# Kernel optimization log

Measured on AMD Instinct MI355X. Metric: run time of the kernel, lower is better.

Reference implementation:

```python
import jax, jax.numpy as jnp
import numpy as np

B, N, EDGES = 16, 50000, 1600000
CLAMP_MIN, CLAMP_MAX = -10.0, 10.0
EPS = 1e-6


def setup_inputs() -> dict:
    key = jax.random.key(0)
    ks = jax.random.split(key, 8)
    return {
        "chem_influence": jax.random.normal(ks[0], (B, N), dtype=jnp.float32),
        "E": jax.random.normal(ks[1], (B, N), dtype=jnp.float32),
        "o_pre": jax.random.uniform(ks[2], (B, N), dtype=jnp.float32),
        "w": jax.random.normal(ks[3], (EDGES,), dtype=jnp.float32),
        "threshold": jax.random.uniform(ks[4], (N,), dtype=jnp.float32),
        "decay": jax.random.uniform(ks[5], (N,), dtype=jnp.float32),
        "src": jax.random.randint(ks[6], (EDGES,), 0, N, dtype=jnp.int32),
        "dst": jax.random.randint(ks[7], (EDGES,), 0, N, dtype=jnp.int32),
    }


def reference(chem_influence, E, o_pre, w, threshold, decay, src, dst):
    # Gap-junction currents: gather, sign-compare, weighted scatter-add.
    Oj = o_pre[:, src]                      # (B, EDGES) presynaptic outputs
    En = E[:, dst]                          # (B, EDGES) postsynaptic internal states
    sgn = jnp.where(Oj >= En, 1.0, -1.0)
    contrib = Oj * w * sgn                  # (B, EDGES)
    gj_sum = jnp.zeros_like(chem_influence).at[:, dst].add(contrib)  # (B, N)

    # Neuron dynamics (eqs 10, 11).
    S = jnp.clip(E + chem_influence + gj_sum, CLAMP_MIN, CLAMP_MAX)
    gt = S > threshold                      # broadcast (N,) over (B, N)
    mask = (~gt) & (jnp.abs(S - E) <= EPS)
    new_o = jax.nn.relu(S - threshold)
    new_e = jnp.where(gt, new_o, jnp.where(mask, E - decay, S))
    return (new_o, new_e)
```

## Files before the change

### kernel.cpp

```cpp
#include <hip/hip_runtime.h>

#define BATCH 16
#define NNODES 50000
#define NEDGES 1600000
#define BN (BATCH * NNODES)
#define NBLK 196
#define EPB 8192
#define BSZ 128
#define NBINS 391
#define CAPE 4992
#define CLAMP_LO -10.0f
#define CLAMP_HI 10.0f
#define EPS_V 1e-6f

__global__ void prep_hist_kernel(const float* __restrict__ o_pre,
                                 const float* __restrict__ E,
                                 const int* __restrict__ dst,
                                 float* __restrict__ o_t,
                                 float* __restrict__ E_t,
                                 int* __restrict__ hist) {
    __shared__ int lh[NBINS];
    const int tid = threadIdx.x, bid = blockIdx.x;
    for (int i = tid; i < NBINS; i += 256) lh[i] = 0;

    int t = bid * 256 + tid;
    if (t < NNODES) {
        float v[BATCH], u[BATCH];
#pragma unroll
        for (int b = 0; b < BATCH; ++b) {
            v[b] = o_pre[b * NNODES + t];
            u[b] = E[b * NNODES + t];
        }
        float4* op = (float4*)(o_t + (size_t)t * BATCH);
        float4* ep = (float4*)(E_t + (size_t)t * BATCH);
#pragma unroll
        for (int k = 0; k < 4; ++k) {
            op[k] = make_float4(v[4 * k], v[4 * k + 1], v[4 * k + 2], v[4 * k + 3]);
            ep[k] = make_float4(u[4 * k], u[4 * k + 1], u[4 * k + 2], u[4 * k + 3]);
        }
    }
    __syncthreads();

    const int4* dst4 = (const int4*)dst;
    const int e4base = bid * (EPB / 4);
#pragma unroll
    for (int j = 0; j < 8; ++j) {
        int i4 = e4base + j * 256 + tid;
        if (i4 * 4 < NEDGES) {
            int4 d4 = dst4[i4];
            atomicAdd(&lh[d4.x >> 7], 1);
            atomicAdd(&lh[d4.y >> 7], 1);
            atomicAdd(&lh[d4.z >> 7], 1);
            atomicAdd(&lh[d4.w >> 7], 1);
        }
    }
    __syncthreads();
    for (int i = tid; i < NBINS; i += 256) hist[i * NBLK + bid] = lh[i];
}

__global__ void scanA_kernel(int* __restrict__ hist, int* __restrict__ totals) {
    __shared__ int sm[256];
    int k = blockIdx.x, t = threadIdx.x;
    int v = (t < NBLK) ? hist[k * NBLK + t] : 0;
    sm[t] = v;
    __syncthreads();
    for (int off = 1; off < 256; off <<= 1) {
        int a = (t >= off) ? sm[t - off] : 0;
        __syncthreads();
        sm[t] += a;
        __syncthreads();
    }
    if (t < NBLK) hist[k * NBLK + t] = sm[t] - v;
    if (t == 0) totals[k] = sm[255];
}

__global__ void scatterA_kernel(const int* __restrict__ src,
                                const int* __restrict__ dst,
                                const float* __restrict__ w,
                                const int* __restrict__ hist,
                                uint2* __restrict__ binned) {
    __shared__ int cur[NBINS];
    const int tid = threadIdx.x, bid = blockIdx.x;
    for (int i = tid; i < NBINS; i += 256)
        cur[i] = i * CAPE + hist[i * NBLK + bid];
    __syncthreads();
    const int4*   dst4 = (const int4*)dst;
    const int4*   src4 = (const int4*)src;
    const float4* w4   = (const float4*)w;
    const int e4base = bid * (EPB / 4);
#pragma unroll
    for (int j = 0; j < 8; ++j) {
        int i4 = e4base + j * 256 + tid;
        if (i4 * 4 < NEDGES) {
            int4 d4 = dst4[i4];
            int4 s4 = src4[i4];
            float4 ww = w4[i4];
            int dd[4] = {d4.x, d4.y, d4.z, d4.w};
            int ss[4] = {s4.x, s4.y, s4.z, s4.w};
            float wv[4] = {ww.x, ww.y, ww.z, ww.w};
#pragma unroll
            for (int m = 0; m < 4; ++m) {
                int d = dd[m];
                int bin = d >> 7;
                int pos = atomicAdd(&cur[bin], 1);
                if (pos < (bin + 1) * CAPE)
                    binned[pos] = make_uint2(
                        (unsigned)ss[m] | ((unsigned)(d & 127) << 16),
                        __float_as_uint(wv[m]));
            }
        }
    }
}

__global__ __launch_bounds__(512) void bin_gather2(
    const float* __restrict__ o_t,
    const float* __restrict__ E_t,
    const float* __restrict__ chem,
    const float* __restrict__ threshold,
    const float* __restrict__ decay,
    const int* __restrict__ totals,
    const uint2* __restrict__ binned,
    float* __restrict__ out_o,
    float* __restrict__ out_e) {
    __shared__ int   cnt_l[BSZ];
    __shared__ int   offs[BSZ + 1];
    __shared__ int   sc[BSZ];
    __shared__ uint2 eb[CAPE];

    const int k = blockIdx.x, tid = threadIdx.x;
    const int node0 = k * BSZ;
    const int nn = (NNODES - node0 < BSZ) ? (NNODES - node0) : BSZ;
    const int s0 = k * CAPE;
    int cnt = totals[k];
    if (cnt > CAPE) cnt = CAPE;
    const int s1 = s0 + cnt;

    if (tid < BSZ) cnt_l[tid] = 0;
    __syncthreads();
    for (int i = s0 + tid; i < s1; i += 512)
        atomicAdd(&cnt_l[(binned[i].x >> 16) & 127], 1);
    __syncthreads();

    if (tid < BSZ) sc[tid] = cnt_l[tid];
    __syncthreads();
    for (int o = 1; o < BSZ; o <<= 1) {
        int v = (tid >= o && tid < BSZ) ? sc[tid - o] : 0;
        __syncthreads();
        if (tid < BSZ) sc[tid] += v;
        __syncthreads();
    }
    if (tid < BSZ) {
        int ex = sc[tid] - cnt_l[tid];
        offs[tid] = ex;
        cnt_l[tid] = ex;
    }
    if (tid == 0) offs[BSZ] = cnt;
    __syncthreads();

    for (int i = s0 + tid; i < s1; i += 512) {
        uint2 p = binned[i];
        int pos = atomicAdd(&cnt_l[(p.x >> 16) & 127], 1);
        if (pos < CAPE) eb[pos] = p;
    }
    __syncthreads();

    for (int t = tid; t < nn * 4; t += 512) {
        int n = t >> 2;
        int q = (t & 3) * 4;
        int gn = node0 + n;
        int e0 = offs[n], e1 = offs[n + 1];
        float4 en = *(const float4*)(E_t + (size_t)gn * BATCH + q);
        float4 acc = make_float4(0.f, 0.f, 0.f, 0.f);
        for (int i = e0; i < e1; ++i) {
            uint2 p = eb[i];
            float wv = __uint_as_float(p.y);
            int s = (int)(p.x & 0xFFFFu);
            float4 oj = *(const float4*)(o_t + (size_t)s * BATCH + q);
            acc.x += (oj.x >= en.x) ? oj.x * wv : -oj.x * wv;
            acc.y += (oj.y >= en.y) ? oj.y * wv : -oj.y * wv;
            acc.z += (oj.z >= en.z) ? oj.z * wv : -oj.z * wv;
            acc.w += (oj.w >= en.w) ? oj.w * wv : -oj.w * wv;
        }
        float th = threshold[gn];
        float dc = decay[gn];
        float ev[4] = {en.x, en.y, en.z, en.w};
        float av[4] = {acc.x, acc.y, acc.z, acc.w};
#pragma unroll
        for (int j = 0; j < 4; ++j) {
            int b = q + j;
            float e = ev[j];
            float S = e + chem[b * NNODES + gn] + av[j];
            S = fminf(fmaxf(S, CLAMP_LO), CLAMP_HI);
            float no = fmaxf(S - th, 0.0f);
            float ne;
            if (S > th) ne = no;
            else if (fabsf(S - e) <= EPS_V) ne = e - dc;
            else ne = S;
            out_o[b * NNODES + gn] = no;
            out_e[b * NNODES + gn] = ne;
        }
    }
}

__global__ void edge_scatter_dev(const float* __restrict__ o_pre, const float* __restrict__ E,
                                 const float* __restrict__ w, const int* __restrict__ src,
                                 const int* __restrict__ dst, float* __restrict__ gj) {
    int e = blockIdx.x * blockDim.x + threadIdx.x;
    if (e >= NEDGES) return;
    int s = src[e];
    int d = dst[e];
    float wv = w[e];
#pragma unroll
    for (int b = 0; b < BATCH; ++b) {
        float oj = o_pre[b * NNODES + s];
        float en = E[b * NNODES + d];
        atomicAdd(&gj[b * NNODES + d], (oj >= en) ? oj * wv : -oj * wv);
    }
}

__global__ void finalize_dev(const float* __restrict__ chem, const float* __restrict__ E,
                             const float* __restrict__ threshold, const float* __restrict__ decay,
                             float* __restrict__ out_o, float* __restrict__ out_e_gj) {
    int i = blockIdx.x * blockDim.x + threadIdx.x;
    if (i >= BN) return;
    int n = i % NNODES;
    float e = E[i];
    float S = e + chem[i] + out_e_gj[i];
    S = fminf(fmaxf(S, CLAMP_LO), CLAMP_HI);
    float th = threshold[n];
    float no = fmaxf(S - th, 0.0f);
    float ne;
    if (S > th) ne = no;
    else if (fabsf(S - e) <= EPS_V) ne = e - decay[n];
    else ne = S;
    out_o[i] = no;
    out_e_gj[i] = ne;
}

extern "C" void kernel_launch(void* const* d_in, const int* in_sizes, int n_in,
                              void* d_out, int out_size, void* d_ws, size_t ws_size,
                              hipStream_t stream) {
    const float* chem      = (const float*)d_in[0];
    const float* E         = (const float*)d_in[1];
    const float* o_pre     = (const float*)d_in[2];
    const float* w         = (const float*)d_in[3];
    const float* threshold = (const float*)d_in[4];
    const float* decay     = (const float*)d_in[5];
    const int*   src       = (const int*)d_in[6];
    const int*   dst       = (const int*)d_in[7];

    float* out_o = (float*)d_out;
    float* out_e = (float*)d_out + BN;

    const size_t OT_OFF  = 0;
    const size_t ET_OFF  = 3200000;
    const size_t BIN_OFF = 6400000;
    const size_t H_OFF   = 22014976;
    const size_t TOT_OFF = 22321536;
    const size_t need    = TOT_OFF + (size_t)NBINS * sizeof(int);

    if (ws_size >= need) {
        char* ws = (char*)d_ws;
        float* o_t    = (float*)(ws + OT_OFF);
        float* E_t    = (float*)(ws + ET_OFF);
        uint2* binned = (uint2*)(ws + BIN_OFF);
        int*   hist   = (int*)(ws + H_OFF);
        int*   totals = (int*)(ws + TOT_OFF);

        prep_hist_kernel<<<NBLK, 256, 0, stream>>>(o_pre, E, dst, o_t, E_t, hist);
        scanA_kernel<<<NBINS, 256, 0, stream>>>(hist, totals);
        scatterA_kernel<<<NBLK, 256, 0, stream>>>(src, dst, w, hist, binned);
        bin_gather2<<<NBINS, 512, 0, stream>>>(o_t, E_t, chem, threshold, decay,
                                               totals, binned, out_o, out_e);
    } else {
        hipMemsetAsync(out_e, 0, (size_t)BN * sizeof(float), stream);
        edge_scatter_dev<<<(NEDGES + 255) / 256, 256, 0, stream>>>(o_pre, E, w, src, dst, out_e);
        finalize_dev<<<(BN + 255) / 256, 256, 0, stream>>>(chem, E, threshold, decay, out_o, out_e);
    }
}
```

Before: 132.3 us.

## Fuse four-kernel binning pipeline into one persistent kernel with grid barriers

Replaces the histogram, scan, scatter and gather kernels with a single persistent kernel of 782 blocks that syncs through software grid barriers on global atomic counters. Bins shrink to 64 nodes each, and E is kept transposed in shared memory rather than written to a workspace. The aim is to remove three kernel launch gaps and the E_t round trip. The cost is spin-wait barriers and a per-call occupancy query on the host. It relies on all blocks being co-resident, which the occupancy check only partly guards, and the hist matrix is much larger (782x782).

```diff
diff --git a/kernel.cpp b/kernel.cpp
--- a/kernel.cpp
+++ b/kernel.cpp
@@ -4,14 +4,211 @@
 #define NNODES 50000
 #define NEDGES 1600000
 #define BN (BATCH * NNODES)
+#define CLAMP_LO -10.0f
+#define CLAMP_HI 10.0f
+#define EPS_V 1e-6f
+
+#define GRID2 782
+#define BSZ2 64
+#define CAPE2 2560
+#define EPB2 2048
+
 #define NBLK 196
 #define EPB 8192
 #define BSZ 128
 #define NBINS 391
 #define CAPE 4992
-#define CLAMP_LO -10.0f
-#define CLAMP_HI 10.0f
-#define EPS_V 1e-6f
+
+__device__ __forceinline__ void grid_barrier(int* ctr) {
+    __syncthreads();
+    if (threadIdx.x == 0) {
+        __threadfence();
+        atomicAdd(ctr, 1);
+        while (__hip_atomic_load(ctr, __ATOMIC_RELAXED, __HIP_MEMORY_SCOPE_AGENT) < GRID2) {
+            __builtin_amdgcn_s_sleep(1);
+        }
+        __threadfence();
+    }
+    __syncthreads();
+}
+
+__global__ __launch_bounds__(256, 4) void fused_all(
+    const float* __restrict__ o_pre, const float* __restrict__ E,
+    const int* __restrict__ src, const int* __restrict__ dst,
+    const float* __restrict__ w, const float* __restrict__ chem,
+    const float* __restrict__ threshold, const float* __restrict__ decay,
+    float* __restrict__ o_t, uint2* __restrict__ binned,
+    int* __restrict__ hist, int* __restrict__ totals, int* __restrict__ bars,
+    float* __restrict__ out_o, float* __restrict__ out_e) {
+    __shared__ __align__(16) char smem_raw[21264];
+    __shared__ float Et_l[BSZ2 * BATCH];
+    int*   lh    = (int*)smem_raw;
+    int*   sm    = (int*)smem_raw;
+    int*   cur   = (int*)smem_raw;
+    uint2* eb    = (uint2*)smem_raw;
+    int*   cnt_l = (int*)(smem_raw + 20480);
+    int*   offs  = (int*)(smem_raw + 20736);
+    int*   sc    = (int*)(smem_raw + 20996);
+
+    const int k = blockIdx.x, tid = threadIdx.x;
+    const int node0 = k * BSZ2;
+    const int nn = (NNODES - node0 < BSZ2) ? (NNODES - node0) : BSZ2;
+
+    for (int i = tid; i < GRID2; i += 256) lh[i] = 0;
+    for (int i = tid; i < BSZ2 * BATCH; i += 256) {
+        int b = i >> 6, n = i & 63;
+        if (n < nn) {
+            o_t[(size_t)(node0 + n) * BATCH + b] = o_pre[b * NNODES + node0 + n];
+            Et_l[n * BATCH + b] = E[b * NNODES + node0 + n];
+        }
+    }
+    __syncthreads();
+    const int4* dst4 = (const int4*)dst;
+#pragma unroll
+    for (int j = 0; j < 2; ++j) {
+        int i4 = k * (EPB2 / 4) + j * 256 + tid;
+        if (i4 * 4 < NEDGES) {
+            int4 d4 = dst4[i4];
+            atomicAdd(&lh[d4.x >> 6], 1);
+            atomicAdd(&lh[d4.y >> 6], 1);
+            atomicAdd(&lh[d4.z >> 6], 1);
+            atomicAdd(&lh[d4.w >> 6], 1);
+        }
+    }
+    __syncthreads();
+    for (int i = tid; i < GRID2; i += 256) hist[(size_t)i * GRID2 + k] = lh[i];
+    grid_barrier(&bars[0]);
+
+    {
+        int* row = hist + (size_t)k * GRID2;
+        int base = tid * 4;
+        int v[4];
+        int psum = 0;
+#pragma unroll
+        for (int j = 0; j < 4; ++j) {
+            int idx = base + j;
+            v[j] = (idx < GRID2) ? row[idx] : 0;
+            psum += v[j];
+        }
+        sm[tid] = psum;
+        __syncthreads();
+        for (int off = 1; off < 256; off <<= 1) {
+            int a = (tid >= off) ? sm[tid - off] : 0;
+            __syncthreads();
+            sm[tid] += a;
+            __syncthreads();
+        }
+        int run = (tid > 0) ? sm[tid - 1] : 0;
+#pragma unroll
+        for (int j = 0; j < 4; ++j) {
+            int idx = base + j;
+            if (idx < GRID2) { row[idx] = run; run += v[j]; }
+        }
+        if (tid == 0) totals[k] = sm[255];
+    }
+    grid_barrier(&bars[1]);
+
+    for (int i = tid; i < GRID2; i += 256)
+        cur[i] = i * CAPE2 + hist[(size_t)i * GRID2 + k];
+    __syncthreads();
+    {
+        const int4*   src4 = (const int4*)src;
+        const float4* w4   = (const float4*)w;
+#pragma unroll
+        for (int j = 0; j < 2; ++j) {
+            int i4 = k * (EPB2 / 4) + j * 256 + tid;
+            if (i4 * 4 < NEDGES) {
+                int4 d4 = dst4[i4];
+                int4 s4 = src4[i4];
+                float4 ww = w4[i4];
+                int dd[4] = {d4.x, d4.y, d4.z, d4.w};
+                int ss[4] = {s4.x, s4.y, s4.z, s4.w};
+                float wv[4] = {ww.x, ww.y, ww.z, ww.w};
+#pragma unroll
+                for (int m = 0; m < 4; ++m) {
+                    int d = dd[m];
+                    int bin = d >> 6;
+                    int pos = atomicAdd(&cur[bin], 1);
+                    if (pos < (bin + 1) * CAPE2)
+                        binned[pos] = make_uint2(
+                            (unsigned)ss[m] | ((unsigned)(d & 63) << 16),
+                            __float_as_uint(wv[m]));
+                }
+            }
+        }
+    }
+    grid_barrier(&bars[2]);
+
+    const int s0 = k * CAPE2;
+    int cnt = totals[k];
+    if (cnt > CAPE2) cnt = CAPE2;
+    const int s1 = s0 + cnt;
+
+    if (tid < BSZ2) cnt_l[tid] = 0;
+    __syncthreads();
+    for (int i = s0 + tid; i < s1; i += 256)
+        atomicAdd(&cnt_l[(binned[i].x >> 16) & 63], 1);
+    __syncthreads();
+    if (tid < BSZ2) sc[tid] = cnt_l[tid];
+    __syncthreads();
+    for (int o = 1; o < BSZ2; o <<= 1) {
+        int v = (tid >= o && tid < BSZ2) ? sc[tid - o] : 0;
+        __syncthreads();
+        if (tid < BSZ2) sc[tid] += v;
+        __syncthreads();
+    }
+    if (tid < BSZ2) {
+        int ex = sc[tid] - cnt_l[tid];
+        offs[tid] = ex;
+        cnt_l[tid] = ex;
+    }
+    if (tid == 0) offs[BSZ2] = cnt;
+    __syncthreads();
+    for (int i = s0 + tid; i < s1; i += 256) {
+        uint2 p = binned[i];
+        int pos = atomicAdd(&cnt_l[(p.x >> 16) & 63], 1);
+        if (pos < CAPE2) eb[pos] = p;
+    }
+    __syncthreads();
+
+    if (tid < nn * 4) {
+        int n = tid >> 2;
+        int q = (tid & 3) * 4;
+        int gn = node0 + n;
+        int e0 = offs[n], e1 = offs[n + 1];
+        float4 en = *(const float4*)(Et_l + n * BATCH + q);
+        float4 acc = make_float4(0.f, 0.f, 0.f, 0.f);
+        for (int i = e0; i < e1; ++i) {
+            uint2 p = eb[i];
+            float wv = __uint_as_float(p.y);
+            int s = (int)(p.x & 0xFFFFu);
+            float4 oj = *(const float4*)(o_t + (size_t)s * BATCH + q);
+            acc.x += (oj.x >= en.x) ? oj.x * wv : -oj.x * wv;
+            acc.y += (oj.y >= en.y) ? oj.y * wv : -oj.y * wv;
+            acc.z += (oj.z >= en.z) ? oj.z * wv : -oj.z * wv;
+            acc.w += (oj.w >= en.w) ? oj.w * wv : -oj.w * wv;
+        }
+        float th = threshold[gn];
+        float dc = decay[gn];
+        float ev[4] = {en.x, en.y, en.z, en.w};
+        float av[4] = {acc.x, acc.y, acc.z, acc.w};
+#pragma unroll
+        for (int j = 0; j < 4; ++j) {
+            int b = q + j;
+            float e = ev[j];
+            float S = e + chem[b * NNODES + gn] + av[j];
+            S = fminf(fmaxf(S, CLAMP_LO), CLAMP_HI);
+            float no = fmaxf(S - th, 0.0f);
+            float ne;
+            if (S > th) ne = no;
+            else if (fabsf(S - e) <= EPS_V) ne = e - dc;
+            else ne = S;
+            out_o[b * NNODES + gn] = no;
+            out_e[b * NNODES + gn] = ne;
+        }
+    }
+}
+
 
 __global__ void prep_hist_kernel(const float* __restrict__ o_pre,
                                  const float* __restrict__ E,
@@ -22,7 +219,6 @@
     __shared__ int lh[NBINS];
     const int tid = threadIdx.x, bid = blockIdx.x;
     for (int i = tid; i < NBINS; i += 256) lh[i] = 0;
-
     int t = bid * 256 + tid;
     if (t < NNODES) {
         float v[BATCH], u[BATCH];
@@ -34,13 +230,12 @@
         float4* op = (float4*)(o_t + (size_t)t * BATCH);
         float4* ep = (float4*)(E_t + (size_t)t * BATCH);
 #pragma unroll
-        for (int k = 0; k < 4; ++k) {
-            op[k] = make_float4(v[4 * k], v[4 * k + 1], v[4 * k + 2], v[4 * k + 3]);
-            ep[k] = make_float4(u[4 * k], u[4 * k + 1], u[4 * k + 2], u[4 * k + 3]);
-        }
-    }
-    __syncthreads();
-
+        for (int kk = 0; kk < 4; ++kk) {
+            op[kk] = make_float4(v[4 * kk], v[4 * kk + 1], v[4 * kk + 2], v[4 * kk + 3]);
+            ep[kk] = make_float4(u[4 * kk], u[4 * kk + 1], u[4 * kk + 2], u[4 * kk + 3]);
+        }
+    }
+    __syncthreads();
     const int4* dst4 = (const int4*)dst;
     const int e4base = bid * (EPB / 4);
 #pragma unroll
@@ -113,20 +308,15 @@
 }
 
 __global__ __launch_bounds__(512) void bin_gather2(
-    const float* __restrict__ o_t,
-    const float* __restrict__ E_t,
-    const float* __restrict__ chem,
-    const float* __restrict__ threshold,
-    const float* __restrict__ decay,
-    const int* __restrict__ totals,
+    const float* __restrict__ o_t, const float* __restrict__ E_t,
+    const float* __restrict__ chem, const float* __restrict__ threshold,
+    const float* __restrict__ decay, const int* __restrict__ totals,
     const uint2* __restrict__ binned,
-    float* __restrict__ out_o,
-    float* __restrict__ out_e) {
+    float* __restrict__ out_o, float* __restrict__ out_e) {
     __shared__ int   cnt_l[BSZ];
     __shared__ int   offs[BSZ + 1];
     __shared__ int   sc[BSZ];
     __shared__ uint2 eb[CAPE];
-
     const int k = blockIdx.x, tid = threadIdx.x;
     const int node0 = k * BSZ;
     const int nn = (NNODES - node0 < BSZ) ? (NNODES - node0) : BSZ;
@@ -134,13 +324,11 @@
     int cnt = totals[k];
     if (cnt > CAPE) cnt = CAPE;
     const int s1 = s0 + cnt;
-
     if (tid < BSZ) cnt_l[tid] = 0;
     __syncthreads();
     for (int i = s0 + tid; i < s1; i += 512)
         atomicAdd(&cnt_l[(binned[i].x >> 16) & 127], 1);
     __syncthreads();
-
     if (tid < BSZ) sc[tid] = cnt_l[tid];
     __syncthreads();
     for (int o = 1; o < BSZ; o <<= 1) {
@@ -156,14 +344,12 @@
     }
     if (tid == 0) offs[BSZ] = cnt;
     __syncthreads();
-
     for (int i = s0 + tid; i < s1; i += 512) {
         uint2 p = binned[i];
         int pos = atomicAdd(&cnt_l[(p.x >> 16) & 127], 1);
         if (pos < CAPE) eb[pos] = p;
     }
     __syncthreads();
-
     for (int t = tid; t < nn * 4; t += 512) {
         int n = t >> 2;
         int q = (t & 3) * 4;
@@ -252,21 +438,42 @@
     float* out_o = (float*)d_out;
     float* out_e = (float*)d_out + BN;
 
+    const size_t F_OT  = 0;
+    const size_t F_BIN = 3200000;
+    const size_t F_H   = 19215360;
+    const size_t F_TOT = 21661456;
+    const size_t F_BAR = 21664592;
+    const size_t need_f = F_BAR + 16;
+
     const size_t OT_OFF  = 0;
     const size_t ET_OFF  = 3200000;
     const size_t BIN_OFF = 6400000;
     const size_t H_OFF   = 22014976;
     const size_t TOT_OFF = 22321536;
-    const size_t need    = TOT_OFF + (size_t)NBINS * sizeof(int);
-
-    if (ws_size >= need) {
+    const size_t need2   = TOT_OFF + (size_t)NBINS * sizeof(int);
+
+    int blocksPerCU = 0;
+    hipError_t oe = hipOccupancyMaxActiveBlocksPerMultiprocessor(&blocksPerCU, fused_all, 256, 0);
+    bool coop_ok = (oe == hipSuccess) && ((long)blocksPerCU * 256 >= GRID2) && (ws_size >= need_f);
+
+    if (coop_ok) {
+        char* ws = (char*)d_ws;
+        float* o_t    = (float*)(ws + F_OT);
+        uint2* binned = (uint2*)(ws + F_BIN);
+        int*   hist   = (int*)(ws + F_H);
+        int*   totals = (int*)(ws + F_TOT);
+        int*   bars   = (int*)(ws + F_BAR);
+        hipMemsetAsync(bars, 0, 3 * sizeof(int), stream);
+        fused_all<<<GRID2, 256, 0, stream>>>(o_pre, E, src, dst, w, chem,
+                                             threshold, decay, o_t, binned,
+                                             hist, totals, bars, out_o, out_e);
+    } else if (ws_size >= need2) {
         char* ws = (char*)d_ws;
         float* o_t    = (float*)(ws + OT_OFF);
         float* E_t    = (float*)(ws + ET_OFF);
         uint2* binned = (uint2*)(ws + BIN_OFF);
         int*   hist   = (int*)(ws + H_OFF);
         int*   totals = (int*)(ws + TOT_OFF);
-
         prep_hist_kernel<<<NBLK, 256, 0, stream>>>(o_pre, E, dst, o_t, E_t, hist);
         scanA_kernel<<<NBINS, 256, 0, stream>>>(hist, totals);
         scatterA_kernel<<<NBLK, 256, 0, stream>>>(src, dst, w, hist, binned);
```

Measured after the change: 433.8 us. +228.0%, slower.

## Fuse histogram, scan and scatter into one kernel using global atomic bin cursors

Applied to the files above, without the earlier changes.

Merges the prep/histogram, scan and scatter kernels into a single kernel. Each block builds a local bin histogram and reserves its slice of every bin with one global atomicAdd, which removes the separate exclusive-scan pass and the second read of dst. Bins shrink from 128 to 64 nodes, giving twice as many gather blocks with 256 threads each. In exchange the order of edges within a bin becomes nondeterministic, so float summation order can vary between runs, and a memset of the counters is added.

```diff
diff --git a/kernel.cpp b/kernel.cpp
--- a/kernel.cpp
+++ b/kernel.cpp
@@ -4,27 +4,33 @@
 #define NNODES 50000
 #define NEDGES 1600000
 #define BN (BATCH * NNODES)
-#define NBLK 196
-#define EPB 8192
-#define BSZ 128
-#define NBINS 391
-#define CAPE 4992
 #define CLAMP_LO -10.0f
 #define CLAMP_HI 10.0f
 #define EPS_V 1e-6f
 
-__global__ void prep_hist_kernel(const float* __restrict__ o_pre,
-                                 const float* __restrict__ E,
-                                 const int* __restrict__ dst,
-                                 float* __restrict__ o_t,
-                                 float* __restrict__ E_t,
-                                 int* __restrict__ hist) {
+#define NBINS 782
+#define BSZ 64
+#define CAPE 2560
+#define K1B 250
+#define EPB 6400
+#define E4PB 1600
+#define NPT 200
+
+__global__ __launch_bounds__(256) void prep_scatter(
+    const float* __restrict__ o_pre, const float* __restrict__ E,
+    const int* __restrict__ src, const int* __restrict__ dst,
+    const float* __restrict__ w,
+    float* __restrict__ o_t, float* __restrict__ E_t,
+    int* __restrict__ cnt,
+    uint2* __restrict__ binned) {
     __shared__ int lh[NBINS];
+    __shared__ int cur[NBINS];
     const int tid = threadIdx.x, bid = blockIdx.x;
+
     for (int i = tid; i < NBINS; i += 256) lh[i] = 0;
 
-    int t = bid * 256 + tid;
-    if (t < NNODES) {
+    if (tid < NPT) {
+        int t = bid * NPT + tid;
         float v[BATCH], u[BATCH];
 #pragma unroll
         for (int b = 0; b < BATCH; ++b) {
@@ -42,86 +48,58 @@
     __syncthreads();
 
     const int4* dst4 = (const int4*)dst;
-    const int e4base = bid * (EPB / 4);
-#pragma unroll
-    for (int j = 0; j < 8; ++j) {
-        int i4 = e4base + j * 256 + tid;
-        if (i4 * 4 < NEDGES) {
-            int4 d4 = dst4[i4];
-            atomicAdd(&lh[d4.x >> 7], 1);
-            atomicAdd(&lh[d4.y >> 7], 1);
-            atomicAdd(&lh[d4.z >> 7], 1);
-            atomicAdd(&lh[d4.w >> 7], 1);
-        }
-    }
-    __syncthreads();
-    for (int i = tid; i < NBINS; i += 256) hist[i * NBLK + bid] = lh[i];
-}
-
-__global__ void scanA_kernel(int* __restrict__ hist, int* __restrict__ totals) {
-    __shared__ int sm[256];
-    int k = blockIdx.x, t = threadIdx.x;
-    int v = (t < NBLK) ? hist[k * NBLK + t] : 0;
-    sm[t] = v;
-    __syncthreads();
-    for (int off = 1; off < 256; off <<= 1) {
-        int a = (t >= off) ? sm[t - off] : 0;
-        __syncthreads();
-        sm[t] += a;
-        __syncthreads();
-    }
-    if (t < NBLK) hist[k * NBLK + t] = sm[t] - v;
-    if (t == 0) totals[k] = sm[255];
-}
-
-__global__ void scatterA_kernel(const int* __restrict__ src,
-                                const int* __restrict__ dst,
-                                const float* __restrict__ w,
-                                const int* __restrict__ hist,
-                                uint2* __restrict__ binned) {
-    __shared__ int cur[NBINS];
-    const int tid = threadIdx.x, bid = blockIdx.x;
-    for (int i = tid; i < NBINS; i += 256)
-        cur[i] = i * CAPE + hist[i * NBLK + bid];
-    __syncthreads();
-    const int4*   dst4 = (const int4*)dst;
+    const int i40 = bid * E4PB;
+#pragma unroll
+    for (int j = 0; j < 7; ++j) {
+        int idx = j * 256 + tid;
+        if (idx < E4PB) {
+            int4 d4 = dst4[i40 + idx];
+            atomicAdd(&lh[d4.x >> 6], 1);
+            atomicAdd(&lh[d4.y >> 6], 1);
+            atomicAdd(&lh[d4.z >> 6], 1);
+            atomicAdd(&lh[d4.w >> 6], 1);
+        }
+    }
+    __syncthreads();
+
+    for (int i = tid; i < NBINS; i += 256) {
+        int c = lh[i];
+        cur[i] = i * CAPE + (c ? atomicAdd(&cnt[i], c) : 0);
+    }
+    __syncthreads();
+
     const int4*   src4 = (const int4*)src;
     const float4* w4   = (const float4*)w;
-    const int e4base = bid * (EPB / 4);
-#pragma unroll
-    for (int j = 0; j < 8; ++j) {
-        int i4 = e4base + j * 256 + tid;
-        if (i4 * 4 < NEDGES) {
-            int4 d4 = dst4[i4];
-            int4 s4 = src4[i4];
-            float4 ww = w4[i4];
+#pragma unroll
+    for (int j = 0; j < 7; ++j) {
+        int idx = j * 256 + tid;
+        if (idx < E4PB) {
+            int4 d4 = dst4[i40 + idx];
+            int4 s4 = src4[i40 + idx];
+            float4 ww = w4[i40 + idx];
             int dd[4] = {d4.x, d4.y, d4.z, d4.w};
             int ss[4] = {s4.x, s4.y, s4.z, s4.w};
             float wv[4] = {ww.x, ww.y, ww.z, ww.w};
 #pragma unroll
             for (int m = 0; m < 4; ++m) {
                 int d = dd[m];
-                int bin = d >> 7;
+                int bin = d >> 6;
                 int pos = atomicAdd(&cur[bin], 1);
                 if (pos < (bin + 1) * CAPE)
                     binned[pos] = make_uint2(
-                        (unsigned)ss[m] | ((unsigned)(d & 127) << 16),
+                        (unsigned)ss[m] | ((unsigned)(d & 63) << 16),
                         __float_as_uint(wv[m]));
             }
         }
     }
 }
 
-__global__ __launch_bounds__(512) void bin_gather2(
-    const float* __restrict__ o_t,
-    const float* __restrict__ E_t,
-    const float* __restrict__ chem,
-    const float* __restrict__ threshold,
-    const float* __restrict__ decay,
-    const int* __restrict__ totals,
+__global__ __launch_bounds__(256) void bin_gather2(
+    const float* __restrict__ o_t, const float* __restrict__ E_t,
+    const float* __restrict__ chem, const float* __restrict__ threshold,
+    const float* __restrict__ decay, const int* __restrict__ cnt,
     const uint2* __restrict__ binned,
-    float* __restrict__ out_o,
-    float* __restrict__ out_e) {
+    float* __restrict__ out_o, float* __restrict__ out_e) {
     __shared__ int   cnt_l[BSZ];
     __shared__ int   offs[BSZ + 1];
     __shared__ int   sc[BSZ];
@@ -131,14 +109,14 @@
     const int node0 = k * BSZ;
     const int nn = (NNODES - node0 < BSZ) ? (NNODES - node0) : BSZ;
     const int s0 = k * CAPE;
-    int cnt = totals[k];
-    if (cnt > CAPE) cnt = CAPE;
-    const int s1 = s0 + cnt;
+    int c = cnt[k];
+    if (c > CAPE) c = CAPE;
+    const int s1 = s0 + c;
 
     if (tid < BSZ) cnt_l[tid] = 0;
     __syncthreads();
-    for (int i = s0 + tid; i < s1; i += 512)
-        atomicAdd(&cnt_l[(binned[i].x >> 16) & 127], 1);
+    for (int i = s0 + tid; i < s1; i += 256)
+        atomicAdd(&cnt_l[(binned[i].x >> 16) & 63], 1);
     __syncthreads();
 
     if (tid < BSZ) sc[tid] = cnt_l[tid];
@@ -154,19 +132,19 @@
         offs[tid] = ex;
         cnt_l[tid] = ex;
     }
-    if (tid == 0) offs[BSZ] = cnt;
-    __syncthreads();
-
-    for (int i = s0 + tid; i < s1; i += 512) {
+    if (tid == 0) offs[BSZ] = c;
+    __syncthreads();
+
+    for (int i = s0 + tid; i < s1; i += 256) {
         uint2 p = binned[i];
-        int pos = atomicAdd(&cnt_l[(p.x >> 16) & 127], 1);
+        int pos = atomicAdd(&cnt_l[(p.x >> 16) & 63], 1);
         if (pos < CAPE) eb[pos] = p;
     }
     __syncthreads();
 
-    for (int t = tid; t < nn * 4; t += 512) {
-        int n = t >> 2;
-        int q = (t & 3) * 4;
+    if (tid < nn * 4) {
+        int n = tid >> 2;
+        int q = (tid & 3) * 4;
         int gn = node0 + n;
         int e0 = offs[n], e1 = offs[n + 1];
         float4 en = *(const float4*)(E_t + (size_t)gn * BATCH + q);
@@ -255,23 +233,21 @@
     const size_t OT_OFF  = 0;
     const size_t ET_OFF  = 3200000;
     const size_t BIN_OFF = 6400000;
-    const size_t H_OFF   = 22014976;
-    const size_t TOT_OFF = 22321536;
-    const size_t need    = TOT_OFF + (size_t)NBINS * sizeof(int);
+    const size_t CNT_OFF = 22415360;
+    const size_t need    = CNT_OFF + (size_t)NBINS * sizeof(int);
 
     if (ws_size >= need) {
         char* ws = (char*)d_ws;
         float* o_t    = (float*)(ws + OT_OFF);
         float* E_t    = (float*)(ws + ET_OFF);
         uint2* binned = (uint2*)(ws + BIN_OFF);
-        int*   hist   = (int*)(ws + H_OFF);
-        int*   totals = (int*)(ws + TOT_OFF);
-
-        prep_hist_kernel<<<NBLK, 256, 0, stream>>>(o_pre, E, dst, o_t, E_t, hist);
-        scanA_kernel<<<NBINS, 256, 0, stream>>>(hist, totals);
-        scatterA_kernel<<<NBLK, 256, 0, stream>>>(src, dst, w, hist, binned);
-        bin_gather2<<<NBINS, 512, 0, stream>>>(o_t, E_t, chem, threshold, decay,
-                                               totals, binned, out_o, out_e);
+        int*   cnt    = (int*)(ws + CNT_OFF);
+
+        hipMemsetAsync(cnt, 0, (size_t)NBINS * sizeof(int), stream);
+        prep_scatter<<<K1B, 256, 0, stream>>>(o_pre, E, src, dst, w,
+                                              o_t, E_t, cnt, binned);
+        bin_gather2<<<NBINS, 256, 0, stream>>>(o_t, E_t, chem, threshold, decay,
+                                               cnt, binned, out_o, out_e);
     } else {
         hipMemsetAsync(out_e, 0, (size_t)BN * sizeof(float), stream);
         edge_scatter_dev<<<(NEDGES + 255) / 256, 256, 0, stream>>>(o_pre, E, w, src, dst, out_e);
```

After: 140.6 us. 1.06x slower.

## Double block count for histogram/scatter passes and scan two elements per thread

Applied to the files above, without the earlier changes.

Changes the edge partitioning from 196 blocks of 8192 edges to 391 blocks of 4096 edges for the histogram and binning kernels. The node transpose now uses only 128 threads per block. The per-bin scan now handles two block counts per thread to cover the larger histogram, and the workspace offset is moved to fit it. The aim is more blocks across the CUs for the atomic-heavy binning passes, at the cost of a larger histogram and more scan work.

```diff
diff --git a/kernel.cpp b/kernel.cpp
--- a/kernel.cpp
+++ b/kernel.cpp
@@ -4,8 +4,8 @@
 #define NNODES 50000
 #define NEDGES 1600000
 #define BN (BATCH * NNODES)
-#define NBLK 196
-#define EPB 8192
+#define NBLK 391
+#define EPB 4096
 #define BSZ 128
 #define NBINS 391
 #define CAPE 4992
@@ -13,30 +13,31 @@
 #define CLAMP_HI 10.0f
 #define EPS_V 1e-6f
 
-__global__ void prep_hist_kernel(const float* __restrict__ o_pre,
-                                 const float* __restrict__ E,
-                                 const int* __restrict__ dst,
-                                 float* __restrict__ o_t,
-                                 float* __restrict__ E_t,
-                                 int* __restrict__ hist) {
+__global__ __launch_bounds__(256) void prep_hist_kernel(
+    const float* __restrict__ o_pre, const float* __restrict__ E,
+    const int* __restrict__ dst,
+    float* __restrict__ o_t, float* __restrict__ E_t,
+    int* __restrict__ hist) {
     __shared__ int lh[NBINS];
     const int tid = threadIdx.x, bid = blockIdx.x;
     for (int i = tid; i < NBINS; i += 256) lh[i] = 0;
 
-    int t = bid * 256 + tid;
-    if (t < NNODES) {
-        float v[BATCH], u[BATCH];
-#pragma unroll
-        for (int b = 0; b < BATCH; ++b) {
-            v[b] = o_pre[b * NNODES + t];
-            u[b] = E[b * NNODES + t];
-        }
-        float4* op = (float4*)(o_t + (size_t)t * BATCH);
-        float4* ep = (float4*)(E_t + (size_t)t * BATCH);
-#pragma unroll
-        for (int k = 0; k < 4; ++k) {
-            op[k] = make_float4(v[4 * k], v[4 * k + 1], v[4 * k + 2], v[4 * k + 3]);
-            ep[k] = make_float4(u[4 * k], u[4 * k + 1], u[4 * k + 2], u[4 * k + 3]);
+    if (tid < 128) {
+        int t = bid * 128 + tid;
+        if (t < NNODES) {
+            float v[BATCH], u[BATCH];
+#pragma unroll
+            for (int b = 0; b < BATCH; ++b) {
+                v[b] = o_pre[b * NNODES + t];
+                u[b] = E[b * NNODES + t];
+            }
+            float4* op = (float4*)(o_t + (size_t)t * BATCH);
+            float4* ep = (float4*)(E_t + (size_t)t * BATCH);
+#pragma unroll
+            for (int k = 0; k < 4; ++k) {
+                op[k] = make_float4(v[4 * k], v[4 * k + 1], v[4 * k + 2], v[4 * k + 3]);
+                ep[k] = make_float4(u[4 * k], u[4 * k + 1], u[4 * k + 2], u[4 * k + 3]);
+            }
         }
     }
     __syncthreads();
@@ -44,7 +45,7 @@
     const int4* dst4 = (const int4*)dst;
     const int e4base = bid * (EPB / 4);
 #pragma unroll
-    for (int j = 0; j < 8; ++j) {
+    for (int j = 0; j < 4; ++j) {
         int i4 = e4base + j * 256 + tid;
         if (i4 * 4 < NEDGES) {
             int4 d4 = dst4[i4];
@@ -58,11 +59,14 @@
     for (int i = tid; i < NBINS; i += 256) hist[i * NBLK + bid] = lh[i];
 }
 
-__global__ void scanA_kernel(int* __restrict__ hist, int* __restrict__ totals) {
+__global__ __launch_bounds__(256) void scanA_kernel(int* __restrict__ hist,
+                                                    int* __restrict__ totals) {
     __shared__ int sm[256];
-    int k = blockIdx.x, t = threadIdx.x;
-    int v = (t < NBLK) ? hist[k * NBLK + t] : 0;
-    sm[t] = v;
+    const int k = blockIdx.x, t = threadIdx.x;
+    const int base = t * 2;
+    int v0 = (base < NBLK) ? hist[k * NBLK + base] : 0;
+    int v1 = (base + 1 < NBLK) ? hist[k * NBLK + base + 1] : 0;
+    sm[t] = v0 + v1;
     __syncthreads();
     for (int off = 1; off < 256; off <<= 1) {
         int a = (t >= off) ? sm[t - off] : 0;
@@ -70,15 +74,16 @@
         sm[t] += a;
         __syncthreads();
     }
-    if (t < NBLK) hist[k * NBLK + t] = sm[t] - v;
-    if (t == 0) totals[k] = sm[255];
-}
-
-__global__ void scatterA_kernel(const int* __restrict__ src,
-                                const int* __restrict__ dst,
-                                const float* __restrict__ w,
-                                const int* __restrict__ hist,
-                                uint2* __restrict__ binned) {
+    int run = (t > 0) ? sm[t - 1] : 0;
+    if (base < NBLK) { hist[k * NBLK + base] = run; run += v0; }
+    if (base + 1 < NBLK) hist[k * NBLK + base + 1] = run;
+    if (t == 255) totals[k] = sm[255];
+}
+
+__global__ __launch_bounds__(256) void scatterA_kernel(
+    const int* __restrict__ src, const int* __restrict__ dst,
+    const float* __restrict__ w, const int* __restrict__ hist,
+    uint2* __restrict__ binned) {
     __shared__ int cur[NBINS];
     const int tid = threadIdx.x, bid = blockIdx.x;
     for (int i = tid; i < NBINS; i += 256)
@@ -89,7 +94,7 @@
     const float4* w4   = (const float4*)w;
     const int e4base = bid * (EPB / 4);
 #pragma unroll
-    for (int j = 0; j < 8; ++j) {
+    for (int j = 0; j < 4; ++j) {
         int i4 = e4base + j * 256 + tid;
         if (i4 * 4 < NEDGES) {
             int4 d4 = dst4[i4];
@@ -113,20 +118,15 @@
 }
 
 __global__ __launch_bounds__(512) void bin_gather2(
-    const float* __restrict__ o_t,
-    const float* __restrict__ E_t,
-    const float* __restrict__ chem,
-    const float* __restrict__ threshold,
-    const float* __restrict__ decay,
-    const int* __restrict__ totals,
+    const float* __restrict__ o_t, const float* __restrict__ E_t,
+    const float* __restrict__ chem, const float* __restrict__ threshold,
+    const float* __restrict__ decay, const int* __restrict__ totals,
     const uint2* __restrict__ binned,
-    float* __restrict__ out_o,
-    float* __restrict__ out_e) {
+    float* __restrict__ out_o, float* __restrict__ out_e) {
     __shared__ int   cnt_l[BSZ];
     __shared__ int   offs[BSZ + 1];
     __shared__ int   sc[BSZ];
     __shared__ uint2 eb[CAPE];
-
     const int k = blockIdx.x, tid = threadIdx.x;
     const int node0 = k * BSZ;
     const int nn = (NNODES - node0 < BSZ) ? (NNODES - node0) : BSZ;
@@ -140,7 +140,6 @@
     for (int i = s0 + tid; i < s1; i += 512)
         atomicAdd(&cnt_l[(binned[i].x >> 16) & 127], 1);
     __syncthreads();
-
     if (tid < BSZ) sc[tid] = cnt_l[tid];
     __syncthreads();
     for (int o = 1; o < BSZ; o <<= 1) {
@@ -156,7 +155,6 @@
     }
     if (tid == 0) offs[BSZ] = cnt;
     __syncthreads();
-
     for (int i = s0 + tid; i < s1; i += 512) {
         uint2 p = binned[i];
         int pos = atomicAdd(&cnt_l[(p.x >> 16) & 127], 1);
@@ -256,7 +254,7 @@
     const size_t ET_OFF  = 3200000;
     const size_t BIN_OFF = 6400000;
     const size_t H_OFF   = 22014976;
-    const size_t TOT_OFF = 22321536;
+    const size_t TOT_OFF = 22626512;
     const size_t need    = TOT_OFF + (size_t)NBINS * sizeof(int);
 
     if (ws_size >= need) {
```

Result: no change. 130.9 us (-1.1%).
